# Performance work log

Hardware: AMD Instinct MI355X
Metric: run time of the kernel (lower is better)

The kernel has to match this reference:

```python
import jax, jax.numpy as jnp
import numpy as np

B, T, D_MODEL, N_HEADS = 2, 2048, 1024, 16
HEAD_DIM = D_MODEL // N_HEADS          # 64
CODE_SIZE = HEAD_DIM // 4              # 16


def setup_inputs() -> dict:
    key = jax.random.key(0)
    k1, k2, k3, k4 = jax.random.split(key, 4)
    x = jax.random.normal(k1, (B, T, D_MODEL), dtype=jnp.float32)
    # nn.Linear weights (out_features, in_features), fan-in init scale
    w_qkv = jax.random.normal(k2, (3 * D_MODEL, D_MODEL), dtype=jnp.float32) / np.sqrt(D_MODEL)
    w_out = jax.random.normal(k3, (D_MODEL, D_MODEL), dtype=jnp.float32) / np.sqrt(D_MODEL)
    fc_code = jax.random.normal(k4, (1, N_HEADS, CODE_SIZE, HEAD_DIM), dtype=jnp.float32)
    return {"x": x, "w_qkv": w_qkv, "w_out": w_out, "fc_code": fc_code}


def reference(x, w_qkv, w_out, fc_code):
    Bx, Tx, _ = x.shape
    scale = HEAD_DIM ** (-0.5)
    qkv = x @ w_qkv.T                                   # (B,T,3*d_model)
    # split_heads with Hs=head_dim on 3*d_model -> (B, 3*nH, T, Hs), then chunk on head axis
    qkv = qkv.reshape(Bx, Tx, 3 * N_HEADS, HEAD_DIM).transpose(0, 2, 1, 3)
    q, k, v = qkv[:, :N_HEADS], qkv[:, N_HEADS:2 * N_HEADS], qkv[:, 2 * N_HEADS:]
    code = fc_code[0]                                   # (nH, C, Hs)
    q = jnp.einsum('bhtd,hcd->bhtc', q, code) * scale   # (B,H,T,C)
    k = jnp.einsum('bhtd,hcd->bhtc', k, code) * scale
    q = jax.nn.softmax(q, axis=-1) * scale
    # causal branch (mask is None)
    k_exp = jnp.exp(k - jnp.max(k, axis=2, keepdims=True))       # (B,H,T,C)
    k_exp_cumsum = jnp.cumsum(k_exp, axis=2)                      # (B,H,T,C)
    kv_cumsum = jnp.cumsum(jnp.einsum('bhtc,bhtd->bhtcd', k_exp, v), axis=2)  # (B,H,T,C,D)
    kv = kv_cumsum / (k_exp_cumsum[..., None] + 1e-9)
    xo = jnp.einsum('bhtc,bhtcd->bhtd', q, kv)                    # (B,H,T,D)
    xo = xo.transpose(0, 2, 1, 3).reshape(Bx, Tx, D_MODEL)        # cat_heads
    return xo @ w_out.T
```

## Files before the change

kernel.cpp:

```cpp
#include <hip/hip_runtime.h>
#include <math.h>

#define B_    2
#define T_    2048
#define D_    1024
#define H_    16
#define HD_   64
#define C_    16
#define SCALE_ 0.125f
#define L_    128
#define NC_   16
#define NW_   1536

typedef __attribute__((ext_vector_type(8))) short short8;
typedef __attribute__((ext_vector_type(4))) float f32x4;

__device__ inline float b2f(uint32_t u16) {
    return __uint_as_float(u16 << 16);
}
__device__ inline ushort f2b(float f) {
    uint32_t u = __float_as_uint(f);
    return (ushort)((u + 0x7FFFu + ((u >> 16) & 1u)) >> 16);
}
__device__ inline uint32_t pack2(float a, float b) {
    return (uint32_t)f2b(a) | ((uint32_t)f2b(b) << 16);
}
__device__ inline void unpack2(uint32_t w, float& a, float& b) {
    a = b2f(w & 0xffffu); b = __uint_as_float(w & 0xffff0000u);
}
__device__ inline void unpack8(uint4 raw, float* dst) {
    unpack2(raw.x, dst[0], dst[1]);
    unpack2(raw.y, dst[2], dst[3]);
    unpack2(raw.z, dst[4], dst[5]);
    unpack2(raw.w, dst[6], dst[7]);
}
__device__ __forceinline__ void gll16(const ushort* g, ushort* l) {
    __builtin_amdgcn_global_load_lds(
        (const __attribute__((address_space(1))) void*)g,
        (__attribute__((address_space(3))) void*)l, 16, 0, 0);
}

__global__ __launch_bounds__(256)
void prep_inputs_kernel(const float* __restrict__ x, const float* __restrict__ w_qkv,
                        const float* __restrict__ w_out, const float* __restrict__ code,
                        ushort* __restrict__ xb, ushort* __restrict__ WallB,
                        ushort* __restrict__ WoB) {
    const int bid = blockIdx.x;
    if (bid < 3072) {
        const float* in;
        ushort* out;
        int i;
        if (bid < 2048) {
            in = x; out = xb;
            i = bid * 2048 + threadIdx.x * 8;
        } else {
            const int sub = bid - 2048;
            const int isW = sub >> 9;
            in = isW ? w_out : (w_qkv + (size_t)2048 * 1024);
            out = isW ? WoB : (WallB + (size_t)512 * 1024);
            i = (sub & 511) * 2048 + threadIdx.x * 8;
        }
        float4 a = *(const float4*)(in + i);
        float4 b = *(const float4*)(in + i + 4);
        uint4 o;
        o.x = pack2(a.x, a.y); o.y = pack2(a.z, a.w);
        o.z = pack2(b.x, b.y); o.w = pack2(b.z, b.w);
        *(uint4*)(out + i) = o;
    } else {
        const int sub = bid - 3072;
        const int isK = sub >> 8;
        const int row = sub & 255;
        const int h = row >> 4;
        __shared__ float cs[HD_];
        if (threadIdx.x < HD_) cs[threadIdx.x] = code[row * HD_ + threadIdx.x];
        __syncthreads();
        const float* wbase = w_qkv + (size_t)(isK * D_ + h * HD_) * D_;
        ushort* outp = WallB + (size_t)(isK * 256 + row) * D_;
        for (int e = threadIdx.x; e < D_; e += 256) {
            float acc = 0.f;
            #pragma unroll 8
            for (int d = 0; d < HD_; ++d) acc += wbase[(size_t)d * D_ + e] * cs[d];
            outp[e] = f2b(acc * SCALE_);
        }
    }
}

template<int WRITE_BF16>
__global__ __launch_bounds__(256)
void gemm_bf16_kernel(const ushort* __restrict__ A, const ushort* __restrict__ Bw,
                      void* __restrict__ Cv, int M, int N, int K) {
    __shared__ ushort As[2][128 * 64];
    __shared__ ushort Bs[2][128 * 64];
    const int tid  = threadIdx.x;
    const int wave = tid >> 6;
    const int lane = tid & 63;
    const int wr = wave >> 1, wc = wave & 1;

    const int gx = gridDim.x;
    int f = blockIdx.y * gx + blockIdx.x;
    const int nwg = gx * gridDim.y;
    if ((nwg & 7) == 0) f = (f & 7) * (nwg >> 3) + (f >> 3);
    const int row0 = (f / gx) * 128;
    const int col0 = (f % gx) * 128;

    f32x4 acc[4][4];
    #pragma unroll
    for (int m = 0; m < 4; ++m)
        #pragma unroll
        for (int n = 0; n < 4; ++n) acc[m][n] = (f32x4){0.f, 0.f, 0.f, 0.f};

    const int srow = lane >> 3;
    const int kA   = ((lane & 7) ^ srow) << 3;
    const int lane15 = lane & 15;
    const int lhi    = lane >> 4;
    const int axor   = (lane15 & 7) << 4;

    const int NT = K >> 6;

    #pragma unroll
    for (int i = 0; i < 4; ++i) {
        const int seg = wave * 4 + i;
        const int r = seg * 8 + srow;
        gll16(A  + (size_t)(row0 + r) * K + kA, &As[0][seg * 512]);
        gll16(Bw + (size_t)(col0 + r) * K + kA, &Bs[0][seg * 512]);
    }
    __syncthreads();

    for (int it = 0; it < NT; ++it) {
        const int cur = it & 1;
        if (it + 1 < NT) {
            const int kk = (it + 1) << 6;
            #pragma unroll
            for (int i = 0; i < 4; ++i) {
                const int seg = wave * 4 + i;
                const int r = seg * 8 + srow;
                gll16(A  + (size_t)(row0 + r) * K + kk + kA, &As[cur ^ 1][seg * 512]);
                gll16(Bw + (size_t)(col0 + r) * K + kk + kA, &Bs[cur ^ 1][seg * 512]);
            }
        }
        const char* Ab = (const char*)As[cur];
        const char* Bb = (const char*)Bs[cur];
        #pragma unroll
        for (int s = 0; s < 2; ++s) {
            short8 af[4], bf[4];
            #pragma unroll
            for (int m = 0; m < 4; ++m) {
                const int r = wr * 64 + m * 16 + lane15;
                const int off = (r * 128 + s * 64 + lhi * 16) ^ axor;
                af[m] = *(const short8*)(Ab + off);
            }
            #pragma unroll
            for (int n = 0; n < 4; ++n) {
                const int r = wc * 64 + n * 16 + lane15;
                const int off = (r * 128 + s * 64 + lhi * 16) ^ axor;
                bf[n] = *(const short8*)(Bb + off);
            }
            #pragma unroll
            for (int m = 0; m < 4; ++m)
                #pragma unroll
                for (int n = 0; n < 4; ++n)
                    acc[m][n] = __builtin_amdgcn_mfma_f32_16x16x32_bf16(
                        af[m], bf[n], acc[m][n], 0, 0, 0);
        }
        __syncthreads();
    }

    #pragma unroll
    for (int m = 0; m < 4; ++m) {
        #pragma unroll
        for (int n = 0; n < 4; ++n) {
            const int row = row0 + wr * 64 + m * 16 + lhi * 4;
            const int col = col0 + wc * 64 + n * 16 + lane15;
            if (WRITE_BF16) {
                ushort* C = (ushort*)Cv;
                #pragma unroll
                for (int j = 0; j < 4; ++j)
                    C[(size_t)(row + j) * N + col] = f2b(acc[m][n][j]);
            } else {
                float* C = (float*)Cv;
                #pragma unroll
                for (int j = 0; j < 4; ++j)
                    C[(size_t)(row + j) * N + col] = acc[m][n][j];
            }
        }
    }
}

__global__ __launch_bounds__(256)
void prep_attn_kernel(const ushort* __restrict__ qkcv, ushort* __restrict__ vT,
                      float* __restrict__ ke_loc, float* __restrict__ kv_loc) {
    const int bid = blockIdx.x;
    const int chunk = bid & (NC_ - 1);
    const int bh = bid >> 4;
    const int b = bh >> 4, h = bh & 15;
    const int t0 = chunk * L_;
    const int tid = threadIdx.x;
    __shared__ __align__(16) ushort tile[128 * 64];
    __shared__ float ke_s[L_][C_];
    __shared__ float gsum[C_][16];
    char* tB = (char*)tile;

    #pragma unroll
    for (int r = 0; r < 4; ++r) {
        const int idx = r * 2048 + tid * 8;
        const int t = idx >> 6, d0 = idx & 63;
        uint4 raw = *(const uint4*)(qkcv + (size_t)(b * T_ + t0 + t) * NW_ + 512 + h * 64 + d0);
        *(uint4*)(tB + ((t * 128 + d0 * 2) ^ (((t >> 3) & 7) << 4))) = raw;
    }
    {
        const int t = tid >> 1, c0 = (tid & 1) * 8;
        uint4 raw = *(const uint4*)(qkcv + (size_t)(b * T_ + t0 + t) * NW_ + 256 + h * C_ + c0);
        float f[8]; unpack8(raw, f);
        #pragma unroll
        for (int j = 0; j < 8; ++j) ke_s[t][c0 + j] = __expf(f[j]);
    }
    __syncthreads();

    {
        const int d = tid >> 2, tq = tid & 3;
        ushort* obase = vT + ((size_t)bh * 64 + d) * 2048 + t0;
        #pragma unroll
        for (int c8 = 0; c8 < 4; ++c8) {
            const int tA = c8 * 32 + tq * 8;
            uint32_t w[4];
            #pragma unroll
            for (int p = 0; p < 4; ++p) {
                const int tL = tA + p * 2;
                uint32_t lo = *(const ushort*)(tB + ((tL * 128 + d * 2) ^ (((tL >> 3) & 7) << 4)));
                uint32_t hi = *(const ushort*)(tB + (((tL + 1) * 128 + d * 2) ^ ((((tL + 1) >> 3) & 7) << 4)));
                w[p] = lo | (hi << 16);
            }
            uint4 o; o.x = w[0]; o.y = w[1]; o.z = w[2]; o.w = w[3];
            *(uint4*)(obase + tA) = o;
        }
    }

    const int c = tid >> 4;
    const int dg = (tid & 15) << 2;
    float a0 = 0.f, a1 = 0.f, a2 = 0.f, a3 = 0.f;
    for (int t = 0; t < L_; ++t) {
        const float kev = ke_s[t][c];
        uint2 rv = *(const uint2*)(tB + ((t * 128 + dg * 2) ^ (((t >> 3) & 7) << 4)));
        float v0, v1, v2, v3;
        unpack2(rv.x, v0, v1); unpack2(rv.y, v2, v3);
        a0 += kev * v0; a1 += kev * v1; a2 += kev * v2; a3 += kev * v3;
    }
    {
        const int cc = tid & 15, g = tid >> 4;
        float s = 0.f;
        #pragma unroll
        for (int u = 0; u < 8; ++u) s += ke_s[g * 8 + u][cc];
        gsum[cc][g] = s;
    }
    __syncthreads();
    if (tid < C_) {
        float s = 0.f;
        #pragma unroll
        for (int g = 0; g < 16; ++g) s += gsum[tid][g];
        ke_loc[(size_t)bid * C_ + tid] = s;
    }
    *(float4*)(kv_loc + (size_t)bid * 1024 + c * HD_ + dg) = make_float4(a0, a1, a2, a3);
}

__global__ __launch_bounds__(256)
void intra_kernel(const ushort* __restrict__ qkcv, const ushort* __restrict__ vT,
                  const float* __restrict__ ke_loc, const float* __restrict__ kv_loc,
                  ushort* __restrict__ xob) {
    const int bid = blockIdx.x;
    const int chunk = bid & (NC_ - 1);
    const int bh = bid >> 4;
    const int b = bh >> 4, h = bh & 15;
    const int t0 = chunk * L_;
    const int tid = threadIdx.x;
    const int wave = tid >> 6, lane = tid & 63;
    const int l15 = lane & 15, lhi = lane >> 4;

    __shared__ __align__(16) ushort ke_bf[128 * 32];
    __shared__ __align__(16) ushort qn_bf[128 * 32];
    __shared__ __align__(16) ushort Vt_s[64 * 128];
    __shared__ __align__(16) ushort Pl[128 * 128];
    __shared__ __align__(16) ushort S0t[64 * 32];
    __shared__ float kesum_s[128][16];
    __shared__ float gsum[16][16];
    __shared__ float e0s[16];

    char* keB = (char*)ke_bf;
    char* qnB = (char*)qn_bf;
    char* vtB = (char*)Vt_s;
    char* plB = (char*)Pl;
    char* s0B = (char*)S0t;

    {
        const int t = tid >> 1, c0 = (tid & 1) * 8;
        uint4 raw = *(const uint4*)(qkcv + (size_t)(b * T_ + t0 + t) * NW_ + 256 + h * C_ + c0);
        float f[8]; unpack8(raw, f);
        uint4 o;
        o.x = pack2(__expf(f[0]), __expf(f[1]));
        o.y = pack2(__expf(f[2]), __expf(f[3]));
        o.z = pack2(__expf(f[4]), __expf(f[5]));
        o.w = pack2(__expf(f[6]), __expf(f[7]));
        const int swz = ((t >> 1) & 3) << 4;
        *(uint4*)(keB + ((t * 64 + c0 * 2) ^ swz)) = o;
        *(uint4*)(keB + ((t * 64 + 32 + c0 * 2) ^ swz)) = make_uint4(0, 0, 0, 0);
    }
    {
        const int d = tid >> 2, q = tid & 3;
        const ushort* src = vT + ((size_t)bh * 64 + d) * 2048 + t0 + q * 32;
        const int swz = (d & 15) << 4;
        #pragma unroll
        for (int i = 0; i < 4; ++i) {
            uint4 raw = *(const uint4*)(src + i * 8);
            *(uint4*)(vtB + ((d * 256 + q * 64 + i * 16) ^ swz)) = raw;
        }
    }
    {
        const int c = tid >> 4;
        const int d0 = (tid & 15) * 4;
        const float* base = kv_loc + (size_t)(bh * NC_) * 1024 + c * 64 + d0;
        float s0 = 0.f, s1 = 0.f, s2 = 0.f, s3 = 0.f;
        for (int ch = 0; ch < chunk; ++ch) {
            float4 t4 = *(const float4*)(base + ch * 1024);
            s0 += t4.x; s1 += t4.y; s2 += t4.z; s3 += t4.w;
        }
        const float sp[4] = {s0, s1, s2, s3};
        #pragma unroll
        for (int j = 0; j < 4; ++j) {
            const int d = d0 + j;
            const int swz2 = ((d >> 1) & 3) << 4;
            *(ushort*)(s0B + ((d * 64 + c * 2) ^ swz2)) = f2b(sp[j]);
        }
        const int dz = tid >> 2;
        const int off = 32 + (tid & 3) * 8;
        const int swzz = ((dz >> 1) & 3) << 4;
        *(uint2*)(s0B + ((dz * 64 + off) ^ swzz)) = make_uint2(0, 0);
    }
    if (tid < 16) {
        float s = 0.f;
        for (int ch = 0; ch < chunk; ++ch)
            s += ke_loc[(size_t)(bh * NC_ + ch) * C_ + tid];
        e0s[tid] = s;
    }
    __syncthreads();

    {
        const int cc = tid & 15, g = tid >> 4;
        float s = 0.f;
        #pragma unroll
        for (int u = 0; u < 8; ++u) {
            const int t = g * 8 + u;
            s += b2f(*(const ushort*)(keB + ((t * 64 + cc * 2) ^ (((t >> 1) & 3) << 4))));
        }
        gsum[cc][g] = s;
    }
    __syncthreads();
    if (tid < 16) {
        float run = e0s[tid];
        #pragma unroll
        for (int g = 0; g < 16; ++g) { float tmp = gsum[tid][g]; gsum[tid][g] = run; run += tmp; }
    }
    __syncthreads();
    {
        const int cc = tid & 15, g = tid >> 4;
        float run = gsum[cc][g];
        #pragma unroll
        for (int u = 0; u < 8; ++u) {
            const int t = g * 8 + u;
            run += b2f(*(const ushort*)(keB + ((t * 64 + cc * 2) ^ (((t >> 1) & 3) << 4))));
            kesum_s[t][cc] = run;
        }
    }
    __syncthreads();

    if (tid < 128) {
        const int t = tid;
        const ushort* qrow = qkcv + (size_t)(b * T_ + t0 + t) * NW_ + h * C_;
        float qv[16];
        uint4 r0 = *(const uint4*)qrow, r1 = *(const uint4*)(qrow + 8);
        unpack8(r0, qv); unpack8(r1, qv + 8);
        float m = qv[0];
        #pragma unroll
        for (int c = 1; c < 16; ++c) m = fmaxf(m, qv[c]);
        float sum = 0.f;
        #pragma unroll
        for (int c = 0; c < 16; ++c) { qv[c] = __expf(qv[c] - m); sum += qv[c]; }
        const float inv = SCALE_ / sum;
        #pragma unroll
        for (int c = 0; c < 16; ++c) qv[c] = qv[c] * inv / (kesum_s[t][c] + 1e-9f);
        uint4 o0, o1;
        o0.x = pack2(qv[0], qv[1]);   o0.y = pack2(qv[2], qv[3]);
        o0.z = pack2(qv[4], qv[5]);   o0.w = pack2(qv[6], qv[7]);
        o1.x = pack2(qv[8], qv[9]);   o1.y = pack2(qv[10], qv[11]);
        o1.z = pack2(qv[12], qv[13]); o1.w = pack2(qv[14], qv[15]);
        const int swz = ((t >> 1) & 3) << 4;
        *(uint4*)(qnB + ((t * 64) ^ swz)) = o0;
        *(uint4*)(qnB + ((t * 64 + 16) ^ swz)) = o1;
        *(uint4*)(qnB + ((t * 64 + 32) ^ swz)) = make_uint4(0, 0, 0, 0);
        *(uint4*)(qnB + ((t * 64 + 48) ^ swz)) = make_uint4(0, 0, 0, 0);
    }
    __syncthreads();

    #pragma unroll
    for (int sr = 0; sr < 2; ++sr) {
        const int sb = wave * 2 + sr;
        const int s_row = sb * 16 + l15;
        short8 af = *(const short8*)(keB + ((s_row * 64 + lhi * 16) ^ (((s_row >> 1) & 3) << 4)));
        #pragma unroll
        for (int tb = 0; tb < 8; ++tb) {
            f32x4 p = (f32x4){0.f, 0.f, 0.f, 0.f};
            if (tb >= sb) {
                const int t_col = tb * 16 + l15;
                short8 bf = *(const short8*)(qnB + ((t_col * 64 + lhi * 16) ^ (((t_col >> 1) & 3) << 4)));
                p = __builtin_amdgcn_mfma_f32_16x16x32_bf16(af, bf, p, 0, 0, 0);
                if (tb == sb) {
                    #pragma unroll
                    for (int j = 0; j < 4; ++j)
                        p[j] = (lhi * 4 + j > l15) ? 0.f : p[j];
                }
            }
            const int t_g = tb * 16 + l15;
            const int sbase = sb * 16 + lhi * 4;
            const int swz = (t_g & 15) << 4;
            *(uint32_t*)(plB + ((t_g * 256 + sbase * 2) ^ swz)) = pack2(p[0], p[1]);
            *(uint32_t*)(plB + ((t_g * 256 + sbase * 2 + 4) ^ swz)) = pack2(p[2], p[3]);
        }
    }
    __syncthreads();

    f32x4 acc[2][4];
    #pragma unroll
    for (int tt = 0; tt < 2; ++tt)
        #pragma unroll
        for (int dt = 0; dt < 4; ++dt) acc[tt][dt] = (f32x4){0.f, 0.f, 0.f, 0.f};

    const int trow = wave * 32;
    #pragma unroll
    for (int tt = 0; tt < 2; ++tt) {
        const int t_g = trow + tt * 16 + l15;
        short8 aq = *(const short8*)(qnB + ((t_g * 64 + lhi * 16) ^ (((t_g >> 1) & 3) << 4)));
        #pragma unroll
        for (int dt = 0; dt < 4; ++dt) {
            const int d = dt * 16 + l15;
            short8 bs = *(const short8*)(s0B + ((d * 64 + lhi * 16) ^ (((d >> 1) & 3) << 4)));
            acc[tt][dt] = __builtin_amdgcn_mfma_f32_16x16x32_bf16(aq, bs, acc[tt][dt], 0, 0, 0);
        }
        const int pswz = (t_g & 15) << 4;
        #pragma unroll
        for (int kb = 0; kb < 4; ++kb) {
            short8 ap = *(const short8*)(plB + ((t_g * 256 + kb * 64 + lhi * 16) ^ pswz));
            #pragma unroll
            for (int dt = 0; dt < 4; ++dt) {
                const int d = dt * 16 + l15;
                short8 bv = *(const short8*)(vtB + ((d * 256 + kb * 64 + lhi * 16) ^ ((d & 15) << 4)));
                acc[tt][dt] = __builtin_amdgcn_mfma_f32_16x16x32_bf16(ap, bv, acc[tt][dt], 0, 0, 0);
            }
        }
    }

    #pragma unroll
    for (int tt = 0; tt < 2; ++tt) {
        const int tg0 = t0 + trow + tt * 16 + lhi * 4;
        #pragma unroll
        for (int dt = 0; dt < 4; ++dt) {
            const int d = dt * 16 + l15;
            ushort* orow = xob + (size_t)(b * T_ + tg0) * D_ + h * HD_ + d;
            #pragma unroll
            for (int j = 0; j < 4; ++j)
                orow[(size_t)j * D_] = f2b(acc[tt][dt][j]);
        }
    }
}

extern "C" void kernel_launch(void* const* d_in, const int* in_sizes, int n_in,
                              void* d_out, int out_size, void* d_ws, size_t ws_size,
                              hipStream_t stream) {
    const float* x     = (const float*)d_in[0];
    const float* w_qkv = (const float*)d_in[1];
    const float* w_out = (const float*)d_in[2];
    const float* code  = (const float*)d_in[3];
    float* out = (float*)d_out;

    ushort* xb    = (ushort*)d_ws;
    ushort* WallB = xb + (size_t)4096 * 1024;
    ushort* WoB   = WallB + (size_t)1536 * 1024;
    ushort* qkcv  = WoB + (size_t)1024 * 1024;
    ushort* xob   = qkcv + (size_t)4096 * 1536;
    ushort* vT    = xob + (size_t)4096 * 1024;
    float*  ke_loc = (float*)(vT + (size_t)32 * 64 * 2048);
    float*  kv_loc = ke_loc + 512 * 16;

    prep_inputs_kernel<<<3584, 256, 0, stream>>>(x, w_qkv, w_out, code, xb, WallB, WoB);

    gemm_bf16_kernel<1><<<dim3(12, 32), 256, 0, stream>>>(xb, WallB, qkcv, 4096, NW_, 1024);

    prep_attn_kernel<<<512, 256, 0, stream>>>(qkcv, vT, ke_loc, kv_loc);
    intra_kernel<<<512, 256, 0, stream>>>(qkcv, vT, ke_loc, kv_loc, xob);

    gemm_bf16_kernel<0><<<dim3(8, 32), 256, 0, stream>>>(xob, WoB, out, 4096, 1024, 1024);
}
```

Measured before the change: 90.67 us.

## Fuse V transpose into QKV GEMM epilogue and shrink GEMM tiles to 128x64

The QKV GEMM epilogue now writes the V columns straight into the transposed vT layout and keeps only the 512 q/k-code columns in a narrower qkcv buffer. This removes the transpose and shared-memory staging that prep_attn_kernel used to do. The GEMM tile shrinks from 128x128 to 128x64, doubling the grid so more workgroups are in flight. In exchange there is less data reuse per tile, vT writes from the epilogue are scattered 8-byte stores, and prep_attn now reads V directly from global memory.

```diff
diff --git a/kernel.cpp b/kernel.cpp
--- a/kernel.cpp
+++ b/kernel.cpp
@@ -10,7 +10,7 @@
 #define SCALE_ 0.125f
 #define L_    128
 #define NC_   16
-#define NW_   1536
+#define QKP_  512
 
 typedef __attribute__((ext_vector_type(8))) short short8;
 typedef __attribute__((ext_vector_type(4))) float f32x4;
@@ -85,27 +85,27 @@
     }
 }
 
-template<int WRITE_BF16>
+template<int MODE>
 __global__ __launch_bounds__(256)
 void gemm_bf16_kernel(const ushort* __restrict__ A, const ushort* __restrict__ Bw,
-                      void* __restrict__ Cv, int M, int N, int K) {
+                      void* __restrict__ Cv, ushort* __restrict__ vTout,
+                      int M, int N, int K) {
     __shared__ ushort As[2][128 * 64];
-    __shared__ ushort Bs[2][128 * 64];
+    __shared__ ushort Bs[2][64 * 64];
     const int tid  = threadIdx.x;
     const int wave = tid >> 6;
     const int lane = tid & 63;
-    const int wr = wave >> 1, wc = wave & 1;
 
     const int gx = gridDim.x;
     int f = blockIdx.y * gx + blockIdx.x;
     const int nwg = gx * gridDim.y;
     if ((nwg & 7) == 0) f = (f & 7) * (nwg >> 3) + (f >> 3);
     const int row0 = (f / gx) * 128;
-    const int col0 = (f % gx) * 128;
-
-    f32x4 acc[4][4];
-    #pragma unroll
-    for (int m = 0; m < 4; ++m)
+    const int col0 = (f % gx) * 64;
+
+    f32x4 acc[2][4];
+    #pragma unroll
+    for (int m = 0; m < 2; ++m)
         #pragma unroll
         for (int n = 0; n < 4; ++n) acc[m][n] = (f32x4){0.f, 0.f, 0.f, 0.f};
 
@@ -117,46 +117,46 @@
 
     const int NT = K >> 6;
 
-    #pragma unroll
-    for (int i = 0; i < 4; ++i) {
-        const int seg = wave * 4 + i;
-        const int r = seg * 8 + srow;
-        gll16(A  + (size_t)(row0 + r) * K + kA, &As[0][seg * 512]);
-        gll16(Bw + (size_t)(col0 + r) * K + kA, &Bs[0][seg * 512]);
-    }
+    auto STAGE = [&](int buf, int kk) {
+        #pragma unroll
+        for (int i = 0; i < 6; ++i) {
+            const int sg = wave * 6 + i;
+            if (sg < 16) {
+                const int r = sg * 8 + srow;
+                gll16(A + (size_t)(row0 + r) * K + kk + kA, &As[buf][sg * 512]);
+            } else {
+                const int sb = sg - 16;
+                const int r = sb * 8 + srow;
+                gll16(Bw + (size_t)(col0 + r) * K + kk + kA, &Bs[buf][sb * 512]);
+            }
+        }
+    };
+
+    STAGE(0, 0);
     __syncthreads();
 
     for (int it = 0; it < NT; ++it) {
         const int cur = it & 1;
-        if (it + 1 < NT) {
-            const int kk = (it + 1) << 6;
-            #pragma unroll
-            for (int i = 0; i < 4; ++i) {
-                const int seg = wave * 4 + i;
-                const int r = seg * 8 + srow;
-                gll16(A  + (size_t)(row0 + r) * K + kk + kA, &As[cur ^ 1][seg * 512]);
-                gll16(Bw + (size_t)(col0 + r) * K + kk + kA, &Bs[cur ^ 1][seg * 512]);
-            }
-        }
+        if (it + 1 < NT) STAGE(cur ^ 1, (it + 1) << 6);
         const char* Ab = (const char*)As[cur];
         const char* Bb = (const char*)Bs[cur];
         #pragma unroll
         for (int s = 0; s < 2; ++s) {
-            short8 af[4], bf[4];
+            short8 af[2], bf[4];
             #pragma unroll
-            for (int m = 0; m < 4; ++m) {
-                const int r = wr * 64 + m * 16 + lane15;
+            for (int m = 0; m < 2; ++m) {
+                const int r = wave * 32 + m * 16 + lane15;
                 const int off = (r * 128 + s * 64 + lhi * 16) ^ axor;
                 af[m] = *(const short8*)(Ab + off);
             }
             #pragma unroll
             for (int n = 0; n < 4; ++n) {
-                const int r = wc * 64 + n * 16 + lane15;
+                const int r = n * 16 + lane15;
                 const int off = (r * 128 + s * 64 + lhi * 16) ^ axor;
                 bf[n] = *(const short8*)(Bb + off);
             }
             #pragma unroll
-            for (int m = 0; m < 4; ++m)
+            for (int m = 0; m < 2; ++m)
                 #pragma unroll
                 for (int n = 0; n < 4; ++n)
                     acc[m][n] = __builtin_amdgcn_mfma_f32_16x16x32_bf16(
@@ -166,28 +166,43 @@
     }
 
     #pragma unroll
-    for (int m = 0; m < 4; ++m) {
+    for (int m = 0; m < 2; ++m) {
         #pragma unroll
         for (int n = 0; n < 4; ++n) {
-            const int row = row0 + wr * 64 + m * 16 + lhi * 4;
-            const int col = col0 + wc * 64 + n * 16 + lane15;
-            if (WRITE_BF16) {
+            const int row = row0 + wave * 32 + m * 16 + lhi * 4;
+            const int col = col0 + n * 16 + lane15;
+            if (MODE == 0) {
+                float* C = (float*)Cv;
+                #pragma unroll
+                for (int j = 0; j < 4; ++j)
+                    C[(size_t)(row + j) * N + col] = acc[m][n][j];
+            } else if (MODE == 1) {
                 ushort* C = (ushort*)Cv;
                 #pragma unroll
                 for (int j = 0; j < 4; ++j)
                     C[(size_t)(row + j) * N + col] = f2b(acc[m][n][j]);
             } else {
-                float* C = (float*)Cv;
-                #pragma unroll
-                for (int j = 0; j < 4; ++j)
-                    C[(size_t)(row + j) * N + col] = acc[m][n][j];
+                if (col0 < 512) {
+                    ushort* C = (ushort*)Cv;
+                    #pragma unroll
+                    for (int j = 0; j < 4; ++j)
+                        C[(size_t)(row + j) * QKP_ + col] = f2b(acc[m][n][j]);
+                } else {
+                    const int dg = col - 512;
+                    const int h = dg >> 6, d = dg & 63;
+                    const int b = row >> 11;
+                    const int t = row & 2047;
+                    ushort* p = vTout + ((size_t)((b * 16 + h) * 64 + d)) * 2048 + t;
+                    *(uint2*)p = make_uint2(pack2(acc[m][n][0], acc[m][n][1]),
+                                            pack2(acc[m][n][2], acc[m][n][3]));
+                }
             }
         }
     }
 }
 
 __global__ __launch_bounds__(256)
-void prep_attn_kernel(const ushort* __restrict__ qkcv, ushort* __restrict__ vT,
+void prep_attn_kernel(const ushort* __restrict__ qkcv, const ushort* __restrict__ vT,
                       float* __restrict__ ke_loc, float* __restrict__ kv_loc) {
     const int bid = blockIdx.x;
     const int chunk = bid & (NC_ - 1);
@@ -195,56 +210,40 @@
     const int b = bh >> 4, h = bh & 15;
     const int t0 = chunk * L_;
     const int tid = threadIdx.x;
-    __shared__ __align__(16) ushort tile[128 * 64];
     __shared__ float ke_s[L_][C_];
     __shared__ float gsum[C_][16];
-    char* tB = (char*)tile;
-
-    #pragma unroll
-    for (int r = 0; r < 4; ++r) {
-        const int idx = r * 2048 + tid * 8;
-        const int t = idx >> 6, d0 = idx & 63;
-        uint4 raw = *(const uint4*)(qkcv + (size_t)(b * T_ + t0 + t) * NW_ + 512 + h * 64 + d0);
-        *(uint4*)(tB + ((t * 128 + d0 * 2) ^ (((t >> 3) & 7) << 4))) = raw;
-    }
+
     {
         const int t = tid >> 1, c0 = (tid & 1) * 8;
-        uint4 raw = *(const uint4*)(qkcv + (size_t)(b * T_ + t0 + t) * NW_ + 256 + h * C_ + c0);
+        uint4 raw = *(const uint4*)(qkcv + (size_t)(b * T_ + t0 + t) * QKP_ + 256 + h * C_ + c0);
         float f[8]; unpack8(raw, f);
         #pragma unroll
         for (int j = 0; j < 8; ++j) ke_s[t][c0 + j] = __expf(f[j]);
     }
     __syncthreads();
 
-    {
-        const int d = tid >> 2, tq = tid & 3;
-        ushort* obase = vT + ((size_t)bh * 64 + d) * 2048 + t0;
-        #pragma unroll
-        for (int c8 = 0; c8 < 4; ++c8) {
-            const int tA = c8 * 32 + tq * 8;
-            uint32_t w[4];
-            #pragma unroll
-            for (int p = 0; p < 4; ++p) {
-                const int tL = tA + p * 2;
-                uint32_t lo = *(const ushort*)(tB + ((tL * 128 + d * 2) ^ (((tL >> 3) & 7) << 4)));
-                uint32_t hi = *(const ushort*)(tB + (((tL + 1) * 128 + d * 2) ^ ((((tL + 1) >> 3) & 7) << 4)));
-                w[p] = lo | (hi << 16);
-            }
-            uint4 o; o.x = w[0]; o.y = w[1]; o.z = w[2]; o.w = w[3];
-            *(uint4*)(obase + tA) = o;
-        }
-    }
-
-    const int c = tid >> 4;
-    const int dg = (tid & 15) << 2;
+    const int d = tid & 63;
+    const int cw = tid >> 6;
+    const ushort* vrow = vT + ((size_t)(bh * 64 + d)) * 2048 + t0;
     float a0 = 0.f, a1 = 0.f, a2 = 0.f, a3 = 0.f;
-    for (int t = 0; t < L_; ++t) {
-        const float kev = ke_s[t][c];
-        uint2 rv = *(const uint2*)(tB + ((t * 128 + dg * 2) ^ (((t >> 3) & 7) << 4)));
-        float v0, v1, v2, v3;
-        unpack2(rv.x, v0, v1); unpack2(rv.y, v2, v3);
-        a0 += kev * v0; a1 += kev * v1; a2 += kev * v2; a3 += kev * v3;
-    }
+    for (int kb = 0; kb < 16; ++kb) {
+        uint4 raw = *(const uint4*)(vrow + kb * 8);
+        float v8[8]; unpack8(raw, v8);
+        #pragma unroll
+        for (int u = 0; u < 8; ++u) {
+            const int t = kb * 8 + u;
+            a0 += ke_s[t][cw * 4 + 0] * v8[u];
+            a1 += ke_s[t][cw * 4 + 1] * v8[u];
+            a2 += ke_s[t][cw * 4 + 2] * v8[u];
+            a3 += ke_s[t][cw * 4 + 3] * v8[u];
+        }
+    }
+    float* kvb = kv_loc + (size_t)bid * 1024 + d;
+    kvb[(cw * 4 + 0) * 64] = a0;
+    kvb[(cw * 4 + 1) * 64] = a1;
+    kvb[(cw * 4 + 2) * 64] = a2;
+    kvb[(cw * 4 + 3) * 64] = a3;
+
     {
         const int cc = tid & 15, g = tid >> 4;
         float s = 0.f;
@@ -259,7 +258,6 @@
         for (int g = 0; g < 16; ++g) s += gsum[tid][g];
         ke_loc[(size_t)bid * C_ + tid] = s;
     }
-    *(float4*)(kv_loc + (size_t)bid * 1024 + c * HD_ + dg) = make_float4(a0, a1, a2, a3);
 }
 
 __global__ __launch_bounds__(256)
@@ -292,7 +290,7 @@
 
     {
         const int t = tid >> 1, c0 = (tid & 1) * 8;
-        uint4 raw = *(const uint4*)(qkcv + (size_t)(b * T_ + t0 + t) * NW_ + 256 + h * C_ + c0);
+        uint4 raw = *(const uint4*)(qkcv + (size_t)(b * T_ + t0 + t) * QKP_ + 256 + h * C_ + c0);
         float f[8]; unpack8(raw, f);
         uint4 o;
         o.x = pack2(__expf(f[0]), __expf(f[1]));
@@ -373,7 +371,7 @@
 
     if (tid < 128) {
         const int t = tid;
-        const ushort* qrow = qkcv + (size_t)(b * T_ + t0 + t) * NW_ + h * C_;
+        const ushort* qrow = qkcv + (size_t)(b * T_ + t0 + t) * QKP_ + h * C_;
         float qv[16];
         uint4 r0 = *(const uint4*)qrow, r1 = *(const uint4*)(qrow + 8);
         unpack8(r0, qv); unpack8(r1, qv + 8);
@@ -483,17 +481,17 @@
     ushort* WallB = xb + (size_t)4096 * 1024;
     ushort* WoB   = WallB + (size_t)1536 * 1024;
     ushort* qkcv  = WoB + (size_t)1024 * 1024;
-    ushort* xob   = qkcv + (size_t)4096 * 1536;
+    ushort* xob   = qkcv + (size_t)4096 * 512;
     ushort* vT    = xob + (size_t)4096 * 1024;
     float*  ke_loc = (float*)(vT + (size_t)32 * 64 * 2048);
     float*  kv_loc = ke_loc + 512 * 16;
 
     prep_inputs_kernel<<<3584, 256, 0, stream>>>(x, w_qkv, w_out, code, xb, WallB, WoB);
 
-    gemm_bf16_kernel<1><<<dim3(12, 32), 256, 0, stream>>>(xb, WallB, qkcv, 4096, NW_, 1024);
+    gemm_bf16_kernel<2><<<dim3(24, 32), 256, 0, stream>>>(xb, WallB, qkcv, vT, 4096, 1536, 1024);
 
     prep_attn_kernel<<<512, 256, 0, stream>>>(qkcv, vT, ke_loc, kv_loc);
     intra_kernel<<<512, 256, 0, stream>>>(qkcv, vT, ke_loc, kv_loc, xob);
 
-    gemm_bf16_kernel<0><<<dim3(8, 32), 256, 0, stream>>>(xob, WoB, out, 4096, 1024, 1024);
-}
+    gemm_bf16_kernel<0><<<dim3(16, 32), 256, 0, stream>>>(xob, WoB, out, nullptr, 4096, 1024, 1024);
+}
```

Measured after the change: 84.72 us. -6.6%, faster.
